# Kernel tuning notes

Measured on AMD Instinct MI355X. Metric: run time of the kernel, lower is better.

The kernel has to match this reference:

```python
import jax, jax.numpy as jnp
import numpy as np
from jax import lax

D_MODEL, D_STATE, D_CONV, D_INNER, DT_RANK = 1024, 16, 4, 2048, 64
B_SZ, L_SEQ = 2, 4096

def setup_inputs() -> dict:
    key = jax.random.key(0)
    ks = jax.random.split(key, 12)
    s = 0.02
    x = jax.random.normal(ks[0], (B_SZ, L_SEQ, D_MODEL), jnp.float32)
    norm_w = jnp.ones((D_MODEL,), jnp.float32)
    norm_b = jnp.zeros((D_MODEL,), jnp.float32)
    W_in = jax.random.normal(ks[1], (D_MODEL, 2 * D_INNER), jnp.float32) * s
    conv_w = jax.random.normal(ks[2], (D_INNER, 1, D_CONV), jnp.float32) * 0.5
    conv_b = jnp.zeros((D_INNER,), jnp.float32)
    W_x = jax.random.normal(ks[3], (D_INNER, DT_RANK + 2 * D_STATE), jnp.float32) * s
    W_dt = jax.random.normal(ks[4], (DT_RANK, D_INNER), jnp.float32) * s
    # dt bias init as in the torch module: inverse-softplus of dt in [dt_min, dt_max]
    dt_init = jnp.exp(jax.random.uniform(ks[5], (D_INNER,)) * (np.log(0.1) - np.log(0.001)) + np.log(0.001))
    dt_init = jnp.clip(dt_init, 1e-4, None)
    b_dt = dt_init + jnp.log(-jnp.expm1(-dt_init))
    A_log = jnp.log(jnp.broadcast_to(jnp.arange(1, D_STATE + 1, dtype=jnp.float32)[None, :], (D_INNER, D_STATE)))
    D = jnp.ones((D_INNER,), jnp.float32)
    W_out = jax.random.normal(ks[6], (D_INNER, D_MODEL), jnp.float32) * s
    return {"x": x, "norm_w": norm_w, "norm_b": norm_b, "W_in": W_in,
            "conv_w": conv_w, "conv_b": conv_b, "W_x": W_x, "W_dt": W_dt,
            "b_dt": b_dt, "A_log": A_log, "D": D, "W_out": W_out}

def _silu(v):
    return v * jax.nn.sigmoid(v)

def _layernorm(v, w, b, eps=1e-5):
    mu = jnp.mean(v, axis=-1, keepdims=True)
    var = jnp.var(v, axis=-1, keepdims=True)
    return (v - mu) * lax.rsqrt(var + eps) * w + b

def _selective_scan(u, delta, A, Bm, Cm, Dp):
    # u, delta: [B,L,d_inner]; A: [d_inner,N]; Bm, Cm: [B,L,N]; Dp: [d_inner]
    Bb, L, d_inner = u.shape
    N = A.shape[1]

    def step(h, inp):
        dt_t, u_t, B_t, C_t = inp  # [B,d_inner],[B,d_inner],[B,N],[B,N]
        A_bar = jnp.exp(dt_t[..., None] * A)                       # [B,d_inner,N]
        h = A_bar * h + dt_t[..., None] * B_t[:, None, :] * u_t[..., None]
        y = jnp.sum(h * C_t[:, None, :], axis=-1)                  # [B,d_inner]
        return h, y

    h0 = jnp.zeros((Bb, d_inner, N), u.dtype)
    xs = (jnp.swapaxes(delta, 0, 1), jnp.swapaxes(u, 0, 1),
          jnp.swapaxes(Bm, 0, 1), jnp.swapaxes(Cm, 0, 1))
    _, ys = lax.scan(step, h0, xs)          # ys: [L,B,d_inner]
    y = jnp.swapaxes(ys, 0, 1)
    return y + u * Dp[None, None, :]

def reference(x, norm_w, norm_b, W_in, conv_w, conv_b, W_x, W_dt, b_dt, A_log, D, W_out):
    residual = x
    xn = _layernorm(x, norm_w, norm_b)
    xz = xn @ W_in                                      # [B,L,2*d_inner]
    x_ssm, z = jnp.split(xz, 2, axis=-1)
    # depthwise causal conv1d (torch pads both sides then truncates -> left pad)
    xt = jnp.swapaxes(x_ssm, 1, 2)                      # [B,d_inner,L]
    xt = jnp.pad(xt, ((0, 0), (0, 0), (D_CONV - 1, 0)))
    xc = lax.conv_general_dilated(xt, conv_w, window_strides=(1,), padding='VALID',
                                  feature_group_count=D_INNER,
                                  dimension_numbers=('NCH', 'OIH', 'NCH'))
    xc = xc + conv_b[None, :, None]
    x_conv = jnp.swapaxes(_silu(xc), 1, 2)              # [B,L,d_inner]
    x_dbl = x_conv @ W_x                                # [B,L,dt_rank+2N]
    dt_low, B_mat, C_mat = jnp.split(x_dbl, [DT_RANK, DT_RANK + D_STATE], axis=-1)
    delta = jax.nn.softplus(dt_low @ W_dt + b_dt)       # [B,L,d_inner]
    A = -jnp.exp(A_log)
    y = _selective_scan(x_conv, delta, A, B_mat, C_mat, D)
    y = y * _silu(z)
    return residual + y @ W_out
```

## Files before the change

### kernel.cpp

```cpp
#include <hip/hip_runtime.h>

typedef unsigned short u16;
typedef __attribute__((ext_vector_type(8))) __bf16 bf16x8;
typedef __attribute__((ext_vector_type(4))) float f32x4;

#define LSEQ 4096
#define DMODEL 1024
#define DINNER 2048

__device__ __forceinline__ float bf2f(u16 u) {
  union { unsigned u; float f; } v; v.u = ((unsigned)u) << 16; return v.f;
}
__device__ __forceinline__ u16 f2bf(float f) {
  union { float f; unsigned u; } v; v.f = f;
  unsigned r = v.u + 0x7fffu + ((v.u >> 16) & 1u);
  return (u16)(r >> 16);
}
__device__ __forceinline__ void gload_lds16(const void* g, void* l) {
  __builtin_amdgcn_global_load_lds(
      (__attribute__((address_space(1))) void*)(unsigned long long)g,
      (__attribute__((address_space(3))) void*)(unsigned int)(unsigned long long)l,
      16, 0, 0);
}
__device__ __forceinline__ float sigmoidf_(float v) { return 1.f / (1.f + __expf(-v)); }

__device__ __forceinline__ void swz_block(int gx, int& bn, int& bm) {
  int lin = blockIdx.x + gridDim.x * blockIdx.y;
  int q = (gridDim.x * gridDim.y) >> 3;
  int s = (lin & 7) * q + (lin >> 3);
  bn = s % gx;
  bm = s / gx;
}

#define SBAR { __builtin_amdgcn_s_barrier(); __builtin_amdgcn_sched_barrier(0); }

__global__ __launch_bounds__(256) void tc_ln_all(const float* __restrict__ W_in,
                                                 const float* __restrict__ W_x,
                                                 const float* __restrict__ W_dt,
                                                 const float* __restrict__ W_out,
                                                 u16* __restrict__ o0, u16* __restrict__ o1,
                                                 u16* __restrict__ o2, u16* __restrict__ o3,
                                                 const float* __restrict__ x,
                                                 const float* __restrict__ nw,
                                                 const float* __restrict__ nb,
                                                 u16* __restrict__ xn_out) {
  int id = blockIdx.x;
  int t = threadIdx.x;
  if (id >= 6528) {
    int row = id - 6528;
    const float* xr = x + (size_t)row * DMODEL;
    float4 v = ((const float4*)xr)[t];
    float s = v.x + v.y + v.z + v.w;
    float s2 = v.x * v.x + v.y * v.y + v.z * v.z + v.w * v.w;
    for (int off = 32; off; off >>= 1) {
      s += __shfl_down(s, off);
      s2 += __shfl_down(s2, off);
    }
    __shared__ float ls[4], ls2[4];
    int wid = t >> 6;
    if ((t & 63) == 0) { ls[wid] = s; ls2[wid] = s2; }
    __syncthreads();
    s = ls[0] + ls[1] + ls[2] + ls[3];
    s2 = ls2[0] + ls2[1] + ls2[2] + ls2[3];
    float mu = s * (1.f / DMODEL);
    float var = s2 * (1.f / DMODEL) - mu * mu;
    float rs = rsqrtf(var + 1e-5f);
    float4 wv = ((const float4*)nw)[t];
    float4 bv = ((const float4*)nb)[t];
    unsigned p0 = (unsigned)f2bf((v.x - mu) * rs * wv.x + bv.x) |
                  ((unsigned)f2bf((v.y - mu) * rs * wv.y + bv.y) << 16);
    unsigned p1 = (unsigned)f2bf((v.z - mu) * rs * wv.z + bv.z) |
                  ((unsigned)f2bf((v.w - mu) * rs * wv.w + bv.w) << 16);
    ((uint2*)(xn_out + (size_t)row * DMODEL))[t] = make_uint2(p0, p1);
    return;
  }
  __shared__ float tile[32][33];
  const float* in;
  u16* out;
  int K, N, Npad, gx, bx;
  if (id < 4096)      { in = W_in;  out = o0; K = 1024; N = 4096; Npad = 4096; gx = 128; bx = id; }
  else if (id < 4352) { in = W_x;   out = o1; K = 2048; N = 96;   Npad = 128;  gx = 4;   bx = id - 4096; }
  else if (id < 4480) { in = W_dt;  out = o2; K = 64;   N = 2048; Npad = 2048; gx = 64;  bx = id - 4352; }
  else                { in = W_out; out = o3; K = 2048; N = 1024; Npad = 1024; gx = 32;  bx = id - 4480; }
  int n0 = (bx % gx) * 32, k0 = (bx / gx) * 32;
  int tx = t & 31, ty = t >> 5;
  for (int i = ty; i < 32; i += 8) {
    int k = k0 + i, n = n0 + tx;
    tile[i][tx] = (k < K && n < N) ? in[(size_t)k * N + n] : 0.f;
  }
  __syncthreads();
  for (int i = ty; i < 32; i += 8) {
    int n = n0 + i, k = k0 + tx;
    if (n < Npad && k < K) out[(size_t)n * K + k] = f2bf(tile[tx][i]);
  }
}

__device__ __forceinline__ void stage8(const u16* grow0, int ld, int kcol0,
                                       u16* lds_u, int ln) {
  int rr = ln >> 3, kb = ln & 7;
  gload_lds16(grow0 + (size_t)rr * ld + kcol0 + ((kb ^ rr) << 3), lds_u);
}

#define LDA_F(mh, BUF)                                                             \
  _Pragma("unroll") for (int mf = 0; mf < 4; ++mf) {                               \
    av[mf][0] = *(const bf16x8*)(qA0 + (BUF) * 16384 + ((mh) * 64 + mf * 16) * 64); \
    av[mf][1] = *(const bf16x8*)(qA1 + (BUF) * 16384 + ((mh) * 64 + mf * 16) * 64); \
  }

#define LDB_F(nh, BUF)                                                             \
  _Pragma("unroll") for (int nf = 0; nf < 2; ++nf) {                               \
    bb[nh][nf][0] = *(const bf16x8*)(qB0 + (BUF) * 16384 + ((nh) * 32 + nf * 16) * 64); \
    bb[nh][nf][1] = *(const bf16x8*)(qB1 + (BUF) * 16384 + ((nh) * 32 + nf * 16) * 64); \
  }

#define MFMA_Q(mh, nh)                                                             \
  __builtin_amdgcn_s_setprio(1);                                                   \
  _Pragma("unroll") for (int mf = 0; mf < 4; ++mf)                                 \
  _Pragma("unroll") for (int nf = 0; nf < 2; ++nf)                                 \
  _Pragma("unroll") for (int kk = 0; kk < 2; ++kk)                                 \
    acc[(mh) * 4 + mf][(nh) * 2 + nf] = __builtin_amdgcn_mfma_f32_16x16x32_bf16(   \
        av[mf][kk], bb[nh][nf][kk], acc[(mh) * 4 + mf][(nh) * 2 + nf], 0, 0, 0);   \
  __builtin_amdgcn_s_setprio(0);

#define STAGE_A(unit, kt, buf)                                                     \
  _Pragma("unroll") for (int c = 0; c < 2; ++c) {                                  \
    int g = w * 2 + c;                                                             \
    int r0 = ((g < 8) ? g * 8 : (g - 8) * 8 + 128) + (unit) * 64;                  \
    stage8(Ag + (size_t)r0 * ldK, ldK, (kt) * 64, LA + (buf) * 16384 + r0 * 64, ln); \
  }

#define STAGE_B(half, kt, buf)                                                     \
  _Pragma("unroll") for (int c = 0; c < 2; ++c) {                                  \
    int g = w * 2 + c;                                                             \
    int r0 = (g >> 2) * 64 + (half) * 32 + (g & 3) * 8;                            \
    stage8(Bg + (size_t)r0 * ldK, ldK, (kt) * 64, LB + (buf) * 16384 + r0 * 64, ln); \
  }

#define PHASES8P(T_, B0_, B1_)                                                     \
  {                                                                                \
    int kt1 = ((T_) + 1 < NT) ? (T_) + 1 : NT - 1;                                 \
    int kt2 = ((T_) + 2 < NT) ? (T_) + 2 : NT - 1;                                 \
    LDA_F(0, B0_); LDB_F(0, B0_); LDB_F(1, B0_);                                   \
    STAGE_A(1, kt1, B1_);                                                          \
    MFMA_Q(0, 0);                                                                  \
    MFMA_Q(0, 1);                                                                  \
    SBAR                                                                           \
    LDA_F(1, B0_);                                                                 \
    STAGE_A(0, kt2, B0_);                                                          \
    STAGE_B(0, kt2, B0_);                                                          \
    STAGE_B(1, kt2, B0_);                                                          \
    asm volatile("s_waitcnt vmcnt(6)" ::: "memory");                               \
    MFMA_Q(1, 1);                                                                  \
    MFMA_Q(1, 0);                                                                  \
    SBAR                                                                           \
  }

template <int OUT_BF16, int EPI>
__global__ __launch_bounds__(512, 2) void gemm8p(const u16* __restrict__ A,
                                                 const u16* __restrict__ Bt,
                                                 void* __restrict__ Cout,
                                                 const float* __restrict__ aux,
                                                 int M, int N, int K, int cthresh) {
  __shared__ alignas(16) u16 lds[65536];
  u16* LA = lds;
  u16* LB = lds + 32768;
  int t = threadIdx.x;
  int w = t >> 6, ln = t & 63;
  int wm = w >> 2, wn = w & 3;
  int bn, bm;
  swz_block(gridDim.x, bn, bm);
  int lr = ln & 15, lq = ln >> 4, key = ln & 7;
  int ldK = K;
  int NT = K >> 6;
  const u16* Ag = A + (size_t)bm * 256 * ldK;
  const u16* Bg = Bt + (size_t)bn * 256 * ldK;
  const u16* qA0 = LA + (wm * 128 + lr) * 64 + ((lq ^ key) << 3);
  const u16* qA1 = LA + (wm * 128 + lr) * 64 + (((4 + lq) ^ key) << 3);
  const u16* qB0 = LB + (wn * 64 + lr) * 64 + ((lq ^ key) << 3);
  const u16* qB1 = LB + (wn * 64 + lr) * 64 + (((4 + lq) ^ key) << 3);
  f32x4 acc[8][4] = {};
  bf16x8 av[4][2], bb[2][2][2];

  STAGE_A(0, 0, 0); STAGE_B(0, 0, 0); STAGE_B(1, 0, 0); STAGE_A(1, 0, 0);
  int k1 = NT > 1 ? 1 : 0;
  STAGE_A(0, k1, 1); STAGE_B(0, k1, 1); STAGE_B(1, k1, 1);
  asm volatile("s_waitcnt vmcnt(6)" ::: "memory");
  SBAR

  for (int TT = 0; TT < NT; TT += 2) {
    PHASES8P(TT, 0, 1)
    PHASES8P(TT + 1, 1, 0)
  }

  int crow0 = bm * 256 + wm * 128;
  int ccol0 = bn * 256 + wn * 64;
#pragma unroll
  for (int mf = 0; mf < 8; ++mf)
#pragma unroll
    for (int nf = 0; nf < 4; ++nf)
#pragma unroll
      for (int r = 0; r < 4; ++r) {
        int row = crow0 + mf * 16 + lq * 4 + r;
        int col = ccol0 + nf * 16 + lr;
        float v = acc[mf][nf][r];
        if (EPI == 1) v += aux[(size_t)row * N + col];
        if (EPI == 2 && col >= cthresh) v = v * sigmoidf_(v);
        if (OUT_BF16)
          ((u16*)Cout)[(size_t)row * N + col] = f2bf(v);
        else
          ((float*)Cout)[(size_t)row * N + col] = v;
      }
}

#define LDA128(mh, BUF)                                                            \
  _Pragma("unroll") for (int mf2 = 0; mf2 < 2; ++mf2) {                            \
    av[mf2][0] = *(const bf16x8*)(rA0 + (BUF) * 8192 + ((mh) * 32 + mf2 * 16) * 64); \
    av[mf2][1] = *(const bf16x8*)(rA1 + (BUF) * 8192 + ((mh) * 32 + mf2 * 16) * 64); \
  }

#define LDB128(nh, BUF, B_)                                                        \
  _Pragma("unroll") for (int nf2 = 0; nf2 < 2; ++nf2) {                            \
    B_[nf2][0] = *(const bf16x8*)(rB0 + (BUF) * 16384 + ((nh) * 32 + nf2 * 16) * 64); \
    B_[nf2][1] = *(const bf16x8*)(rB1 + (BUF) * 16384 + ((nh) * 32 + nf2 * 16) * 64); \
  }

#define MFMA_Q128(mh, nh, B_)                                                      \
  __builtin_amdgcn_s_setprio(1);                                                   \
  _Pragma("unroll") for (int mf2 = 0; mf2 < 2; ++mf2)                              \
  _Pragma("unroll") for (int nf2 = 0; nf2 < 2; ++nf2)                              \
  _Pragma("unroll") for (int kk = 0; kk < 2; ++kk)                                 \
    acc[(mh) * 2 + mf2][(nh) * 2 + nf2] = __builtin_amdgcn_mfma_f32_16x16x32_bf16( \
        av[mf2][kk], B_[nf2][kk], acc[(mh) * 2 + mf2][(nh) * 2 + nf2], 0, 0, 0);   \
  __builtin_amdgcn_s_setprio(0);

#define STAGE_A128(unit, kt, buf)                                                  \
  {                                                                                \
    int r0 = (w >> 2) * 64 + (unit) * 32 + (w & 3) * 8;                            \
    stage8(Ag + (size_t)r0 * ldK, ldK, (kt) * 64, LA + (buf) * 8192 + r0 * 64, ln); \
  }

#define STAGE_B128(half, kt, buf)                                                  \
  _Pragma("unroll") for (int c = 0; c < 2; ++c) {                                  \
    int g = w * 2 + c;                                                             \
    int r0 = (g >> 2) * 64 + (half) * 32 + (g & 3) * 8;                            \
    stage8(Bg + (size_t)r0 * ldK, ldK, (kt) * 64, LB + (buf) * 16384 + r0 * 64, ln); \
  }

#define PHASES128(T_, B0_, B1_)                                                    \
  {                                                                                \
    int kt1 = ((T_) + 1 < NT) ? (T_) + 1 : NT - 1;                                 \
    int kt2 = ((T_) + 2 < NT) ? (T_) + 2 : NT - 1;                                 \
    LDA128(0, B0_);                                                                \
    LDB128(0, B0_, bbl);                                                           \
    LDB128(1, B0_, bbh);                                                           \
    STAGE_A128(1, kt1, B1_);                                                       \
    MFMA_Q128(0, 0, bbl);                                                          \
    MFMA_Q128(0, 1, bbh);                                                          \
    SBAR                                                                           \
    LDA128(1, B0_);                                                                \
    STAGE_A128(0, kt2, B0_);                                                       \
    STAGE_B128(0, kt2, B0_);                                                       \
    STAGE_B128(1, kt2, B0_);                                                       \
    asm volatile("s_waitcnt vmcnt(5)" ::: "memory");                               \
    MFMA_Q128(1, 1, bbh);                                                          \
    MFMA_Q128(1, 0, bbl);                                                          \
    SBAR                                                                           \
  }

__global__ __launch_bounds__(512, 2) void gemm128_res(const u16* __restrict__ A,
                                                      const u16* __restrict__ Bt,
                                                      float* __restrict__ Cout,
                                                      const float* __restrict__ res,
                                                      int M, int N, int K) {
  __shared__ alignas(16) u16 lds[49152];
  u16* LA = lds;
  u16* LB = lds + 16384;
  int t = threadIdx.x;
  int w = t >> 6, ln = t & 63;
  int wm = w >> 2, wn = w & 3;
  int bn, bm;
  swz_block(gridDim.x, bn, bm);
  int lr = ln & 15, lq = ln >> 4, key = ln & 7;
  int ldK = K;
  int NT = K >> 6;
  const u16* Ag = A + (size_t)bm * 128 * ldK;
  const u16* Bg = Bt + (size_t)bn * 256 * ldK;
  const u16* rA0 = LA + (wm * 64 + lr) * 64 + ((lq ^ key) << 3);
  const u16* rA1 = LA + (wm * 64 + lr) * 64 + (((4 + lq) ^ key) << 3);
  const u16* rB0 = LB + (wn * 64 + lr) * 64 + ((lq ^ key) << 3);
  const u16* rB1 = LB + (wn * 64 + lr) * 64 + (((4 + lq) ^ key) << 3);
  f32x4 acc[4][4] = {};
  bf16x8 av[2][2], bbl[2][2], bbh[2][2];

  STAGE_A128(0, 0, 0); STAGE_B128(0, 0, 0); STAGE_B128(1, 0, 0); STAGE_A128(1, 0, 0);
  int k1 = NT > 1 ? 1 : 0;
  STAGE_A128(0, k1, 1); STAGE_B128(0, k1, 1); STAGE_B128(1, k1, 1);
  asm volatile("s_waitcnt vmcnt(5)" ::: "memory");
  SBAR

  for (int TT = 0; TT < NT; TT += 2) {
    PHASES128(TT, 0, 1)
    PHASES128(TT + 1, 1, 0)
  }

  int crow0 = bm * 128 + wm * 64;
  int ccol0 = bn * 256 + wn * 64;
#pragma unroll
  for (int mf = 0; mf < 4; ++mf)
#pragma unroll
    for (int nf = 0; nf < 4; ++nf)
#pragma unroll
      for (int r = 0; r < 4; ++r) {
        int row = crow0 + mf * 16 + lq * 4 + r;
        int col = ccol0 + nf * 16 + lr;
        Cout[(size_t)row * N + col] = acc[mf][nf][r] + res[(size_t)row * N + col];
      }
}

template <int OUT_BF16, int EPI, int SPLITK>
__global__ __launch_bounds__(256) void gemm_bt(const u16* __restrict__ A,
                                               const u16* __restrict__ Bt,
                                               void* __restrict__ Cout,
                                               const float* __restrict__ aux,
                                               int M, int N, int K, int ld, int cthresh) {
  __shared__ alignas(16) u16 As[128 * 32];
  __shared__ alignas(16) u16 Bs[128 * 32];
  int t = threadIdx.x;
  int w = t >> 6, ln = t & 63;
  int wr = w >> 1, wc = w & 1;
  int bm = blockIdx.y, bn = blockIdx.x;
  int lr = ln & 15, lk = (ln >> 4) * 8;
  f32x4 acc[4][4] = {};
  int kz = SPLITK ? blockIdx.z * K : 0;
  const u16* Abase = A + (size_t)bm * 128 * ld + kz;
  const u16* Bbase = Bt + (size_t)bn * 128 * ld + kz;
  for (int k0 = 0; k0 < K; k0 += 32) {
#pragma unroll
    for (int c = 0; c < 2; ++c) {
      int chunk = w * 2 + c;
      int ee = chunk * 512 + ln * 8;
      int row = ee >> 5, col = ee & 31;
      gload_lds16(Abase + (size_t)row * ld + k0 + col, As + chunk * 512);
      gload_lds16(Bbase + (size_t)row * ld + k0 + col, Bs + chunk * 512);
    }
    __syncthreads();
    bf16x8 af[4], bfr[4];
#pragma unroll
    for (int m = 0; m < 4; ++m)
      af[m] = *(const bf16x8*)(As + (wr * 64 + m * 16 + lr) * 32 + lk);
#pragma unroll
    for (int n = 0; n < 4; ++n)
      bfr[n] = *(const bf16x8*)(Bs + (wc * 64 + n * 16 + lr) * 32 + lk);
#pragma unroll
    for (int m = 0; m < 4; ++m)
#pragma unroll
      for (int n = 0; n < 4; ++n)
        acc[m][n] = __builtin_amdgcn_mfma_f32_16x16x32_bf16(af[m], bfr[n], acc[m][n], 0, 0, 0);
    __syncthreads();
  }
  int rb = bm * 128 + wr * 64 + (ln >> 4) * 4;
  int cb = bn * 128 + wc * 64 + lr;
  float* Cpart = SPLITK ? ((float*)Cout + (size_t)blockIdx.z * M * N) : (float*)Cout;
#pragma unroll
  for (int m = 0; m < 4; ++m)
#pragma unroll
    for (int n = 0; n < 4; ++n)
#pragma unroll
      for (int r = 0; r < 4; ++r) {
        int row = rb + m * 16 + r;
        int col = cb + n * 16;
        float v = acc[m][n][r];
        if (EPI == 3) {
          float dtr = v + aux[col];
          v = dtr > 15.f ? dtr : __logf(1.f + __expf(dtr));
        }
        if (OUT_BF16)
          ((u16*)Cpart)[(size_t)row * N + col] = f2bf(v);
        else
          Cpart[(size_t)row * N + col] = v;
      }
}

__global__ __launch_bounds__(256) void reduce_xdbl(const float* __restrict__ part,
                                                   float* __restrict__ xdbl,
                                                   u16* __restrict__ dtlow) {
  int i = blockIdx.x * 256 + threadIdx.x;
  float s = 0.f;
#pragma unroll
  for (int z = 0; z < 8; ++z) s += part[(size_t)z * (8192 * 128) + i];
  xdbl[i] = s;
  int col = i & 127;
  if (col < 64) dtlow[(size_t)(i >> 7) * 64 + col] = f2bf(s);
}

__global__ __launch_bounds__(256) void conv_silu(const u16* __restrict__ xz,
                                                 const float* __restrict__ cw,
                                                 const float* __restrict__ cb,
                                                 u16* __restrict__ out) {
  int d2 = blockIdx.x * 256 + threadIdx.x;
  int d = d2 * 2;
  int l0 = blockIdx.y * 8;
  int b = blockIdx.z;
  float w0a = cw[d * 4 + 0], w1a = cw[d * 4 + 1], w2a = cw[d * 4 + 2], w3a = cw[d * 4 + 3];
  float w0b = cw[d * 4 + 4], w1b = cw[d * 4 + 5], w2b = cw[d * 4 + 6], w3b = cw[d * 4 + 7];
  float biasa = cb[d], biasb = cb[d + 1];
  const u16* xp = xz + ((size_t)b * LSEQ) * 4096 + d;
  float xa[11], xb[11];
#pragma unroll
  for (int i = 0; i < 11; ++i) {
    int l = l0 - 3 + i;
    unsigned pk = (l >= 0) ? *(const unsigned*)(xp + (size_t)l * 4096) : 0u;
    xa[i] = bf2f((u16)(pk & 0xffffu));
    xb[i] = bf2f((u16)(pk >> 16));
  }
  u16* op = out + ((size_t)b * LSEQ + l0) * DINNER + d;
#pragma unroll
  for (int i = 0; i < 8; ++i) {
    float va = biasa + w0a * xa[i] + w1a * xa[i + 1] + w2a * xa[i + 2] + w3a * xa[i + 3];
    float vb = biasb + w0b * xb[i] + w1b * xb[i + 1] + w2b * xb[i + 2] + w3b * xb[i + 3];
    unsigned pk = (unsigned)f2bf(va * sigmoidf_(va)) |
                  ((unsigned)f2bf(vb * sigmoidf_(vb)) << 16);
    *(unsigned*)(op + (size_t)i * DINNER) = pk;
  }
}

__device__ __forceinline__ void compute_a(float dt, const float* An, bool fast, float* av) {
  if (fast) {
    float q = __expf(-dt);
    float q2 = q * q, q4 = q2 * q2;
    av[0] = q; av[1] = q2; av[2] = q2 * q; av[3] = q4;
#pragma unroll
    for (int n = 4; n < 16; ++n) av[n] = av[n - 4] * q4;
  } else {
#pragma unroll
    for (int n = 0; n < 16; ++n) av[n] = __expf(dt * An[n]);
  }
}

__device__ __forceinline__ void load_An(const float* A_log, int d, float* An, bool& fast) {
  const float4* A4 = (const float4*)(A_log + (size_t)d * 16);
  fast = true;
#pragma unroll
  for (int q = 0; q < 4; ++q) {
    float4 a = A4[q];
    An[q * 4 + 0] = -__expf(a.x);
    An[q * 4 + 1] = -__expf(a.y);
    An[q * 4 + 2] = -__expf(a.z);
    An[q * 4 + 3] = -__expf(a.w);
  }
#pragma unroll
  for (int n = 0; n < 16; ++n)
    fast = fast && (__builtin_fabsf(An[n] + (float)(n + 1)) < 1e-3f * (n + 1));
}

__global__ __launch_bounds__(256) void scan1(const u16* __restrict__ dtbf,
                                             const u16* __restrict__ ubf,
                                             const float* __restrict__ xdbl,
                                             const float* __restrict__ A_log,
                                             float* __restrict__ sdt_out,
                                             u16* __restrict__ H_bf) {
  int d = blockIdx.x * 256 + threadIdx.x;
  int b = blockIdx.y, c = blockIdx.z;
  size_t row0 = (size_t)b * LSEQ + c * 64;
  float An[16];
  bool fast;
  load_An(A_log, d, An, fast);
  const u16* dtp = dtbf + row0 * DINNER + d;
  const u16* up = ubf + row0 * DINNER + d;
  const float* Bp = xdbl + row0 * 128 + 64;
  float h[16];
#pragma unroll
  for (int n = 0; n < 16; ++n) h[n] = 0.f;
  float sdt = 0.f;
  float dt_c = bf2f(dtp[0]);
  float uu_c = bf2f(up[0]);
  const float4* B4 = (const float4*)Bp;
  float4 b0c = B4[0], b1c = B4[1], b2c = B4[2], b3c = B4[3];
  for (int i = 0; i < 64; ++i) {
    float dt_n = dt_c, uu_n = uu_c;
    float4 b0n = b0c, b1n = b1c, b2n = b2c, b3n = b3c;
    if (i < 63) {
      dt_n = bf2f(dtp[(size_t)(i + 1) * DINNER]);
      uu_n = bf2f(up[(size_t)(i + 1) * DINNER]);
      const float4* B4n = (const float4*)(Bp + (size_t)(i + 1) * 128);
      b0n = B4n[0]; b1n = B4n[1]; b2n = B4n[2]; b3n = B4n[3];
    }
    float dtu = dt_c * uu_c;
    sdt += dt_c;
    float Bf[16] = {b0c.x, b0c.y, b0c.z, b0c.w, b1c.x, b1c.y, b1c.z, b1c.w,
                    b2c.x, b2c.y, b2c.z, b2c.w, b3c.x, b3c.y, b3c.z, b3c.w};
    float av[16];
    compute_a(dt_c, An, fast, av);
#pragma unroll
    for (int n = 0; n < 16; ++n) h[n] = av[n] * h[n] + dtu * Bf[n];
    dt_c = dt_n; uu_c = uu_n;
    b0c = b0n; b1c = b1n; b2c = b2n; b3c = b3n;
  }
  int bd = b * DINNER + d;
  sdt_out[(size_t)c * 4096 + bd] = sdt;
  unsigned wds[8];
#pragma unroll
  for (int q = 0; q < 8; ++q)
    wds[q] = (unsigned)f2bf(h[2 * q]) | ((unsigned)f2bf(h[2 * q + 1]) << 16);
  uint4* Hp = (uint4*)(H_bf + (size_t)c * 65536 + (size_t)bd * 16);
  Hp[0] = make_uint4(wds[0], wds[1], wds[2], wds[3]);
  Hp[1] = make_uint4(wds[4], wds[5], wds[6], wds[7]);
}

__global__ __launch_bounds__(256) void scan2(const u16* __restrict__ H_bf,
                                             const float* __restrict__ sdt,
                                             const float* __restrict__ A_log,
                                             u16* __restrict__ Hinit_bf) {
  int i = blockIdx.x * 256 + threadIdx.x;
  int n = i & 15, bd = i >> 4;
  int d = bd & 2047;
  float An = -__expf(A_log[d * 16 + n]);
  float h = 0.f;
  for (int c = 0; c < 64; ++c) {
    Hinit_bf[(size_t)c * 65536 + i] = f2bf(h);
    float p = __expf(An * sdt[(size_t)c * 4096 + bd]);
    h = p * h + bf2f(H_bf[(size_t)c * 65536 + i]);
  }
}

__global__ __launch_bounds__(256) void scan3(const u16* __restrict__ dtbf,
                                             const u16* __restrict__ ubf,
                                             const float* __restrict__ xdbl,
                                             const float* __restrict__ A_log,
                                             const float* __restrict__ Dp,
                                             const u16* __restrict__ xzbf,
                                             const u16* __restrict__ Hinit_bf,
                                             u16* __restrict__ ybf) {
  int d = blockIdx.x * 256 + threadIdx.x;
  int b = blockIdx.y, c = blockIdx.z;
  size_t row0 = (size_t)b * LSEQ + c * 64;
  float An[16];
  bool fast;
  load_An(A_log, d, An, fast);
  const u16* dtp = dtbf + row0 * DINNER + d;
  const u16* up = ubf + row0 * DINNER + d;
  const float* Bp = xdbl + row0 * 128 + 64;
  const float* Cp = xdbl + row0 * 128 + 80;
  const u16* gp = xzbf + row0 * 4096 + DINNER + d;
  u16* yp = ybf + row0 * DINNER + d;
  float Dv = Dp[d];
  float h[16];
  {
    const uint4* Hi4 = (const uint4*)(Hinit_bf + (size_t)c * 65536 +
                                      ((size_t)b * DINNER + d) * 16);
    uint4 p0 = Hi4[0], p1 = Hi4[1];
    unsigned wd[8] = {p0.x, p0.y, p0.z, p0.w, p1.x, p1.y, p1.z, p1.w};
#pragma unroll
    for (int q = 0; q < 8; ++q) {
      h[2 * q] = bf2f((u16)(wd[q] & 0xffffu));
      h[2 * q + 1] = bf2f((u16)(wd[q] >> 16));
    }
  }
  float dt_c = bf2f(dtp[0]);
  float uu_c = bf2f(up[0]);
  float g_c = bf2f(gp[0]);
  const float4* B4 = (const float4*)Bp;
  const float4* C4 = (const float4*)Cp;
  float4 b0c = B4[0], b1c = B4[1], b2c = B4[2], b3c = B4[3];
  float4 c0c = C4[0], c1c = C4[1], c2c = C4[2], c3c = C4[3];
  for (int i = 0; i < 64; ++i) {
    float dt_n = dt_c, uu_n = uu_c, g_n = g_c;
    float4 b0n = b0c, b1n = b1c, b2n = b2c, b3n = b3c;
    float4 c0n = c0c, c1n = c1c, c2n = c2c, c3n = c3c;
    if (i < 63) {
      dt_n = bf2f(dtp[(size_t)(i + 1) * DINNER]);
      uu_n = bf2f(up[(size_t)(i + 1) * DINNER]);
      g_n = bf2f(gp[(size_t)(i + 1) * 4096]);
      const float4* B4n = (const float4*)(Bp + (size_t)(i + 1) * 128);
      const float4* C4n = (const float4*)(Cp + (size_t)(i + 1) * 128);
      b0n = B4n[0]; b1n = B4n[1]; b2n = B4n[2]; b3n = B4n[3];
      c0n = C4n[0]; c1n = C4n[1]; c2n = C4n[2]; c3n = C4n[3];
    }
    float dtu = dt_c * uu_c;
    float Bf[16] = {b0c.x, b0c.y, b0c.z, b0c.w, b1c.x, b1c.y, b1c.z, b1c.w,
                    b2c.x, b2c.y, b2c.z, b2c.w, b3c.x, b3c.y, b3c.z, b3c.w};
    float Cf[16] = {c0c.x, c0c.y, c0c.z, c0c.w, c1c.x, c1c.y, c1c.z, c1c.w,
                    c2c.x, c2c.y, c2c.z, c2c.w, c3c.x, c3c.y, c3c.z, c3c.w};
    float av[16];
    compute_a(dt_c, An, fast, av);
    float y = 0.f;
#pragma unroll
    for (int n = 0; n < 16; ++n) {
      h[n] = av[n] * h[n] + dtu * Bf[n];
      y += h[n] * Cf[n];
    }
    yp[(size_t)i * DINNER] = f2bf((y + uu_c * Dv) * g_c);
    dt_c = dt_n; uu_c = uu_n; g_c = g_n;
    b0c = b0n; b1c = b1n; b2c = b2n; b3c = b3n;
    c0c = c0n; c1c = c1n; c2c = c2n; c3c = c3n;
  }
}

extern "C" void kernel_launch(void* const* d_in, const int* in_sizes, int n_in,
                              void* d_out, int out_size, void* d_ws, size_t ws_size,
                              hipStream_t stream) {
  const float* x = (const float*)d_in[0];
  const float* nw = (const float*)d_in[1];
  const float* nb = (const float*)d_in[2];
  const float* W_in = (const float*)d_in[3];
  const float* convw = (const float*)d_in[4];
  const float* convb = (const float*)d_in[5];
  const float* W_x = (const float*)d_in[6];
  const float* W_dt = (const float*)d_in[7];
  const float* b_dt = (const float*)d_in[8];
  const float* A_log = (const float*)d_in[9];
  const float* Dp = (const float*)d_in[10];
  const float* W_out = (const float*)d_in[11];
  float* out = (float*)d_out;

  char* wp = (char*)d_ws;
  auto alloc = [&](size_t bytes) {
    char* p = wp;
    wp += (bytes + 255) & ~(size_t)255;
    return p;
  };
  u16* xz_bf = (u16*)alloc((size_t)8192 * 4096 * 2);
  u16* xconv_bf = (u16*)alloc((size_t)8192 * 2048 * 2);
  u16* xn_bf = (u16*)alloc((size_t)8192 * 1024 * 2);
  float* xdbl = (float*)alloc((size_t)8192 * 128 * 4);
  u16* dt_bf = (u16*)alloc((size_t)8192 * 2048 * 2);
  u16* dtlow_bf = (u16*)alloc((size_t)8192 * 64 * 2);
  u16* Wint = (u16*)alloc((size_t)4096 * 1024 * 2);
  u16* Wxt = (u16*)alloc((size_t)128 * 2048 * 2);
  u16* Wdtt = (u16*)alloc((size_t)2048 * 64 * 2);
  u16* Woutt = (u16*)alloc((size_t)1024 * 2048 * 2);
  float* P = (float*)alloc((size_t)64 * 65536 * 4);
  float* H = (float*)alloc((size_t)64 * 65536 * 4);
  float* Hinit = (float*)alloc((size_t)64 * 65536 * 4);
  float* xdbl_part = (float*)P;
  float* sdtP = (float*)P;
  u16* H_bf16 = (u16*)H;
  u16* Hinit_bf16 = (u16*)Hinit;
  u16* y_bf = (u16*)P;

  tc_ln_all<<<6528 + 8192, 256, 0, stream>>>(W_in, W_x, W_dt, W_out, Wint, Wxt, Wdtt, Woutt,
                                             x, nw, nb, xn_bf);

  gemm8p<1, 2><<<dim3(16, 32), 512, 0, stream>>>(xn_bf, Wint, xz_bf, nullptr,
                                                 8192, 4096, 1024, 2048);
  conv_silu<<<dim3(4, 512, 2), 256, 0, stream>>>(xz_bf, convw, convb, xconv_bf);
  gemm_bt<0, 0, 1><<<dim3(1, 64, 8), 256, 0, stream>>>(xconv_bf, Wxt, xdbl_part, nullptr,
                                                       8192, 128, 256, 2048, 0);
  reduce_xdbl<<<4096, 256, 0, stream>>>(xdbl_part, xdbl, dtlow_bf);
  gemm_bt<1, 3, 0><<<dim3(16, 64), 256, 0, stream>>>(dtlow_bf, Wdtt, dt_bf, b_dt,
                                                     8192, 2048, 64, 64, 0);
  scan1<<<dim3(8, 2, 64), 256, 0, stream>>>(dt_bf, xconv_bf, xdbl, A_log, sdtP, H_bf16);
  scan2<<<256, 256, 0, stream>>>(H_bf16, sdtP, A_log, Hinit_bf16);
  scan3<<<dim3(8, 2, 64), 256, 0, stream>>>(dt_bf, xconv_bf, xdbl, A_log, Dp, xz_bf,
                                            Hinit_bf16, y_bf);
  gemm128_res<<<dim3(4, 64), 512, 0, stream>>>(y_bf, Woutt, out, x, 8192, 1024, 2048);
}
```

Baseline: 307.3 us.

## Replace in-projection GEMM with 128x256 tile, K=32 pipelined kernel at higher occupancy

The in_proj GEMM kernel moves from a 256x256 tile with K-step 64 and 128 KB LDS to a 128x256 tile with K-step 32 and 48 KB LDS. Launch bounds go from 2 to 4 blocks per CU, and the grid doubles in M to 16x64 blocks. The aim is more occupancy and better latency hiding, plus finer load balance across CUs. The cost is lower arithmetic intensity per block, more barriers per unit of K, and a new XOR swizzle and wait-count schedule that must stay correct.

```diff
diff --git a/kernel.cpp b/kernel.cpp
--- a/kernel.cpp
+++ b/kernel.cpp
@@ -100,102 +100,96 @@
   int rr = ln >> 3, kb = ln & 7;
   gload_lds16(grow0 + (size_t)rr * ld + kcol0 + ((kb ^ rr) << 3), lds_u);
 }
-
-#define LDA_F(mh, BUF)                                                             \
-  _Pragma("unroll") for (int mf = 0; mf < 4; ++mf) {                               \
-    av[mf][0] = *(const bf16x8*)(qA0 + (BUF) * 16384 + ((mh) * 64 + mf * 16) * 64); \
-    av[mf][1] = *(const bf16x8*)(qA1 + (BUF) * 16384 + ((mh) * 64 + mf * 16) * 64); \
-  }
-
-#define LDB_F(nh, BUF)                                                             \
-  _Pragma("unroll") for (int nf = 0; nf < 2; ++nf) {                               \
-    bb[nh][nf][0] = *(const bf16x8*)(qB0 + (BUF) * 16384 + ((nh) * 32 + nf * 16) * 64); \
-    bb[nh][nf][1] = *(const bf16x8*)(qB1 + (BUF) * 16384 + ((nh) * 32 + nf * 16) * 64); \
-  }
-
-#define MFMA_Q(mh, nh)                                                             \
+__device__ __forceinline__ void stage16r(const u16* grow0, int ld, int kcol0,
+                                         u16* lds_u, int ln) {
+  int rr = ln >> 2, kb = ln & 3;
+  gload_lds16(grow0 + (size_t)rr * ld + kcol0 + ((kb ^ ((rr >> 1) & 3)) << 3), lds_u);
+}
+
+#define LDA3(mh, BUF)                                                              \
+  _Pragma("unroll") for (int mf = 0; mf < 2; ++mf)                                 \
+    av3[mf] = *(const bf16x8*)(qA3 + (BUF) * 4096 + ((mh) * 32 + mf * 16) * 32);
+
+#define LDB3(nh, BUF, B_)                                                          \
+  _Pragma("unroll") for (int nf = 0; nf < 2; ++nf)                                 \
+    B_[nf] = *(const bf16x8*)(qB3 + (BUF) * 8192 + ((nh) * 32 + nf * 16) * 32);
+
+#define MFMA_Q3(mh, nh, B_)                                                        \
   __builtin_amdgcn_s_setprio(1);                                                   \
-  _Pragma("unroll") for (int mf = 0; mf < 4; ++mf)                                 \
+  _Pragma("unroll") for (int mf = 0; mf < 2; ++mf)                                 \
   _Pragma("unroll") for (int nf = 0; nf < 2; ++nf)                                 \
-  _Pragma("unroll") for (int kk = 0; kk < 2; ++kk)                                 \
-    acc[(mh) * 4 + mf][(nh) * 2 + nf] = __builtin_amdgcn_mfma_f32_16x16x32_bf16(   \
-        av[mf][kk], bb[nh][nf][kk], acc[(mh) * 4 + mf][(nh) * 2 + nf], 0, 0, 0);   \
+    acc[(mh) * 2 + mf][(nh) * 2 + nf] = __builtin_amdgcn_mfma_f32_16x16x32_bf16(   \
+        av3[mf], B_[nf], acc[(mh) * 2 + mf][(nh) * 2 + nf], 0, 0, 0);              \
   __builtin_amdgcn_s_setprio(0);
 
-#define STAGE_A(unit, kt, buf)                                                     \
-  _Pragma("unroll") for (int c = 0; c < 2; ++c) {                                  \
-    int g = w * 2 + c;                                                             \
-    int r0 = ((g < 8) ? g * 8 : (g - 8) * 8 + 128) + (unit) * 64;                  \
-    stage8(Ag + (size_t)r0 * ldK, ldK, (kt) * 64, LA + (buf) * 16384 + r0 * 64, ln); \
-  }
-
-#define STAGE_B(half, kt, buf)                                                     \
-  _Pragma("unroll") for (int c = 0; c < 2; ++c) {                                  \
-    int g = w * 2 + c;                                                             \
-    int r0 = (g >> 2) * 64 + (half) * 32 + (g & 3) * 8;                            \
-    stage8(Bg + (size_t)r0 * ldK, ldK, (kt) * 64, LB + (buf) * 16384 + r0 * 64, ln); \
-  }
-
-#define PHASES8P(T_, B0_, B1_)                                                     \
+#define STAGE_A3(kt, buf)                                                          \
+  stage16r(Ag + (size_t)(w * 16) * ldK, ldK, (kt) * 32,                            \
+           LA3 + (buf) * 4096 + (w * 16) * 32, ln);
+
+#define STAGE_B3(half, kt, buf)                                                    \
+  stage16r(Bg + (size_t)((half) * 128 + w * 16) * ldK, ldK, (kt) * 32,             \
+           LB3 + (buf) * 8192 + ((half) * 128 + w * 16) * 32, ln);
+
+#define PH3(T_, B0_, B1_)                                                          \
   {                                                                                \
     int kt1 = ((T_) + 1 < NT) ? (T_) + 1 : NT - 1;                                 \
     int kt2 = ((T_) + 2 < NT) ? (T_) + 2 : NT - 1;                                 \
-    LDA_F(0, B0_); LDB_F(0, B0_); LDB_F(1, B0_);                                   \
-    STAGE_A(1, kt1, B1_);                                                          \
-    MFMA_Q(0, 0);                                                                  \
-    MFMA_Q(0, 1);                                                                  \
+    LDA3(0, B0_);                                                                  \
+    LDB3(0, B0_, bbl3);                                                            \
+    __builtin_amdgcn_sched_barrier(0);                                             \
+    LDB3(1, B0_, bbh3);                                                            \
+    STAGE_A3(kt1, B1_);                                                            \
+    MFMA_Q3(0, 0, bbl3);                                                           \
+    MFMA_Q3(0, 1, bbh3);                                                           \
+    LDA3(1, B0_);                                                                  \
     SBAR                                                                           \
-    LDA_F(1, B0_);                                                                 \
-    STAGE_A(0, kt2, B0_);                                                          \
-    STAGE_B(0, kt2, B0_);                                                          \
-    STAGE_B(1, kt2, B0_);                                                          \
-    asm volatile("s_waitcnt vmcnt(6)" ::: "memory");                               \
-    MFMA_Q(1, 1);                                                                  \
-    MFMA_Q(1, 0);                                                                  \
+    STAGE_B3(0, kt2, B0_);                                                         \
+    STAGE_B3(1, kt2, B0_);                                                         \
+    MFMA_Q3(1, 1, bbh3);                                                           \
+    asm volatile("s_waitcnt vmcnt(2)" ::: "memory");                               \
+    MFMA_Q3(1, 0, bbl3);                                                           \
     SBAR                                                                           \
   }
 
 template <int OUT_BF16, int EPI>
-__global__ __launch_bounds__(512, 2) void gemm8p(const u16* __restrict__ A,
-                                                 const u16* __restrict__ Bt,
-                                                 void* __restrict__ Cout,
-                                                 const float* __restrict__ aux,
-                                                 int M, int N, int K, int cthresh) {
-  __shared__ alignas(16) u16 lds[65536];
-  u16* LA = lds;
-  u16* LB = lds + 32768;
+__global__ __launch_bounds__(512, 4) void gemm_k32(const u16* __restrict__ A,
+                                                   const u16* __restrict__ Bt,
+                                                   void* __restrict__ Cout,
+                                                   const float* __restrict__ aux,
+                                                   int M, int N, int K, int cthresh) {
+  __shared__ alignas(16) u16 lds3[24576];
+  u16* LA3 = lds3;
+  u16* LB3 = lds3 + 8192;
   int t = threadIdx.x;
   int w = t >> 6, ln = t & 63;
   int wm = w >> 2, wn = w & 3;
   int bn, bm;
   swz_block(gridDim.x, bn, bm);
-  int lr = ln & 15, lq = ln >> 4, key = ln & 7;
+  int lr = ln & 15, lq = ln >> 4, key3 = (lr >> 1) & 3;
   int ldK = K;
-  int NT = K >> 6;
-  const u16* Ag = A + (size_t)bm * 256 * ldK;
+  int NT = K >> 5;
+  const u16* Ag = A + (size_t)bm * 128 * ldK;
   const u16* Bg = Bt + (size_t)bn * 256 * ldK;
-  const u16* qA0 = LA + (wm * 128 + lr) * 64 + ((lq ^ key) << 3);
-  const u16* qA1 = LA + (wm * 128 + lr) * 64 + (((4 + lq) ^ key) << 3);
-  const u16* qB0 = LB + (wn * 64 + lr) * 64 + ((lq ^ key) << 3);
-  const u16* qB1 = LB + (wn * 64 + lr) * 64 + (((4 + lq) ^ key) << 3);
-  f32x4 acc[8][4] = {};
-  bf16x8 av[4][2], bb[2][2][2];
-
-  STAGE_A(0, 0, 0); STAGE_B(0, 0, 0); STAGE_B(1, 0, 0); STAGE_A(1, 0, 0);
+  const u16* qA3 = LA3 + (wm * 64 + lr) * 32 + ((lq ^ key3) << 3);
+  const u16* qB3 = LB3 + (wn * 64 + lr) * 32 + ((lq ^ key3) << 3);
+  f32x4 acc[4][4] = {};
+  bf16x8 av3[2], bbl3[2], bbh3[2];
+
+  STAGE_A3(0, 0); STAGE_B3(0, 0, 0); STAGE_B3(1, 0, 0);
   int k1 = NT > 1 ? 1 : 0;
-  STAGE_A(0, k1, 1); STAGE_B(0, k1, 1); STAGE_B(1, k1, 1);
-  asm volatile("s_waitcnt vmcnt(6)" ::: "memory");
+  STAGE_B3(0, k1, 1); STAGE_B3(1, k1, 1);
+  asm volatile("s_waitcnt vmcnt(2)" ::: "memory");
   SBAR
 
   for (int TT = 0; TT < NT; TT += 2) {
-    PHASES8P(TT, 0, 1)
-    PHASES8P(TT + 1, 1, 0)
-  }
-
-  int crow0 = bm * 256 + wm * 128;
+    PH3(TT, 0, 1)
+    PH3(TT + 1, 1, 0)
+  }
+
+  int crow0 = bm * 128 + wm * 64;
   int ccol0 = bn * 256 + wn * 64;
 #pragma unroll
-  for (int mf = 0; mf < 8; ++mf)
+  for (int mf = 0; mf < 4; ++mf)
 #pragma unroll
     for (int nf = 0; nf < 4; ++nf)
 #pragma unroll
@@ -641,8 +635,8 @@
   tc_ln_all<<<6528 + 8192, 256, 0, stream>>>(W_in, W_x, W_dt, W_out, Wint, Wxt, Wdtt, Woutt,
                                              x, nw, nb, xn_bf);
 
-  gemm8p<1, 2><<<dim3(16, 32), 512, 0, stream>>>(xn_bf, Wint, xz_bf, nullptr,
-                                                 8192, 4096, 1024, 2048);
+  gemm_k32<1, 2><<<dim3(16, 64), 512, 0, stream>>>(xn_bf, Wint, xz_bf, nullptr,
+                                                   8192, 4096, 1024, 2048);
   conv_silu<<<dim3(4, 512, 2), 256, 0, stream>>>(xz_bf, convw, convb, xconv_bf);
   gemm_bt<0, 0, 1><<<dim3(1, 64, 8), 256, 0, stream>>>(xconv_bf, Wxt, xdbl_part, nullptr,
                                                        8192, 128, 256, 2048, 0);
```

New measurement: 311.9 us. No clear change (+1.5%).
